# Kernel tuning notes

Measured on AMD Instinct MI355X. Metric: run time of the kernel, lower is better.

Reference implementation:

```python
import jax, jax.numpy as jnp
import numpy as np

N_NODES = 100000
N_EDGES = 1600000
IN_DIM, HID_DIM, OUT_DIM = 32, 16, 8


def setup_inputs() -> dict:
    key = jax.random.key(0)
    ks = jax.random.split(key, 10)
    x = jax.random.normal(ks[0], (N_NODES, IN_DIM), dtype=jnp.float32)
    edge_index = jax.random.randint(ks[1], (2, N_EDGES), 0, N_NODES, dtype=jnp.int32)
    s1 = 1.0 / np.sqrt(IN_DIM)
    s2 = 1.0 / np.sqrt(HID_DIM)
    s3 = 1.0 / np.sqrt(OUT_DIM)
    return {
        "x": x,
        "edge_index": edge_index,
        # SAGEConv layer 1: lin_l (neighbor, with bias) and lin_r (root)
        "Wl1": jax.random.uniform(ks[2], (HID_DIM, IN_DIM), jnp.float32, -s1, s1),
        "bl1": jnp.zeros((HID_DIM,), jnp.float32),
        "Wr1": jax.random.uniform(ks[3], (HID_DIM, IN_DIM), jnp.float32, -s1, s1),
        # SAGEConv layer 2
        "Wl2": jax.random.uniform(ks[4], (OUT_DIM, HID_DIM), jnp.float32, -s2, s2),
        "bl2": jnp.zeros((OUT_DIM,), jnp.float32),
        "Wr2": jax.random.uniform(ks[5], (OUT_DIM, HID_DIM), jnp.float32, -s2, s2),
        # final Linear head
        "Wfc": jax.random.uniform(ks[6], (1, OUT_DIM), jnp.float32, -s3, s3),
        "bfc": jax.random.uniform(ks[7], (1,), jnp.float32, -s3, s3),
    }


def _sage_conv(x, src, dst, Wl, bl, Wr):
    # mean-aggregate neighbor messages x[src] at destination nodes
    msg_sum = jax.ops.segment_sum(x[src], dst, num_segments=N_NODES)  # [N, d]
    deg = jax.ops.segment_sum(jnp.ones((src.shape[0],), x.dtype), dst, num_segments=N_NODES)
    mean = msg_sum / jnp.maximum(deg, 1.0)[:, None]
    # out = lin_l(mean_neighbors) + lin_r(x_root)
    return mean @ Wl.T + bl + x @ Wr.T


def reference(x, edge_index, Wl1, bl1, Wr1, Wl2, bl2, Wr2, Wfc, bfc):
    src, dst = edge_index[0], edge_index[1]
    h = _sage_conv(x, src, dst, Wl1, bl1, Wr1)
    h = jax.nn.relu(h)
    h = _sage_conv(h, src, dst, Wl2, bl2, Wr2)
    return h @ Wfc.T + bfc  # [N, 1]
```

## Files before the change

kernel.cpp:

```cpp
#include <hip/hip_runtime.h>

#define NN 100000
#define NE 1600000
#define IN_DIM 32
#define HID_DIM 16
#define OUT_DIM 8

#define NPB 256
#define NBK ((NN + NPB - 1) / NPB)
#define CAP 5632
#define EPB 4096
#define NT_BUCKET ((NE + EPB - 1) / EPB)
#define NT_PRE1 ((NN + 255) / 256)
#define GRID1 (NT_BUCKET + NT_PRE1)
#define BF_STRIDE 16

__global__ __launch_bounds__(256) void k_phase1(
    const float* __restrict__ x, const int* __restrict__ src, const int* __restrict__ dst,
    const float* __restrict__ Wl1, const float* __restrict__ bl1, const float* __restrict__ Wr1,
    const float* __restrict__ Wl2, const float* __restrict__ bl2, const float* __restrict__ Wr2,
    const float* __restrict__ Wfc, const float* __restrict__ bfc,
    int* __restrict__ bucketfill, unsigned int* __restrict__ bucket,
    float* __restrict__ z, float* __restrict__ rb, float* __restrict__ uvc)
{
    __shared__ char smemraw[4800];
    int tid = threadIdx.x;

    if (blockIdx.x < NT_BUCKET) {
        int* lcnt  = (int*)smemraw;
        int* lbase = lcnt + NBK;
        int* lfill = lbase + NBK;
        int e0 = blockIdx.x * EPB;
        int e1 = min(e0 + EPB, NE);
        for (int i = tid; i < NBK; i += 256) lcnt[i] = 0;
        __syncthreads();
        for (int e = e0 + tid; e < e1; e += 256) atomicAdd(&lcnt[dst[e] >> 8], 1);
        __syncthreads();
        for (int i = tid; i < NBK; i += 256) {
            lbase[i] = (lcnt[i] > 0) ? atomicAdd(&bucketfill[i * BF_STRIDE], lcnt[i]) : 0;
            lfill[i] = 0;
        }
        __syncthreads();
        for (int e = e0 + tid; e < e1; e += 256) {
            int d = dst[e], s = src[e];
            int b = d >> 8;
            int p = atomicAdd(&lfill[b], 1);
            bucket[(size_t)b * CAP + lbase[b] + p] =
                (unsigned)(d & (NPB - 1)) | ((unsigned)s << 8);
        }
    } else {
        int chunk = blockIdx.x - NT_BUCKET;
        float* sWl = (float*)smemraw;
        float* sWr = sWl + 512;
        float* sb  = sWr + 512;
        for (int i = tid; i < HID_DIM * IN_DIM; i += 256) {
            sWl[i] = Wl1[i];
            sWr[i] = Wr1[i];
        }
        if (tid < HID_DIM) sb[tid] = bl1[tid];
        if (chunk == 0) {
            if (tid < HID_DIM) {
                float uu = 0.f, vv = 0.f;
#pragma unroll
                for (int o = 0; o < OUT_DIM; o++) {
                    uu += Wfc[o] * Wl2[o * HID_DIM + tid];
                    vv += Wfc[o] * Wr2[o * HID_DIM + tid];
                }
                uvc[tid] = uu;
                uvc[HID_DIM + tid] = vv;
            }
            if (tid == 0) {
                float c0 = bfc[0];
#pragma unroll
                for (int o = 0; o < OUT_DIM; o++) c0 += Wfc[o] * bl2[o];
                uvc[2 * HID_DIM] = c0;
            }
        }
        __syncthreads();
        int n = chunk * 256 + tid;
        if (n < NN) {
            float xv[IN_DIM];
            const float4* x4 = (const float4*)(x + (size_t)n * IN_DIM);
#pragma unroll
            for (int c = 0; c < 8; c++) {
                float4 b = x4[c];
                xv[c * 4 + 0] = b.x; xv[c * 4 + 1] = b.y;
                xv[c * 4 + 2] = b.z; xv[c * 4 + 3] = b.w;
            }
            float zo[HID_DIM], ro[HID_DIM];
#pragma unroll
            for (int o = 0; o < HID_DIM; o++) {
                float az = 0.f, ar = sb[o];
#pragma unroll
                for (int i = 0; i < IN_DIM; i++) {
                    az += sWl[o * IN_DIM + i] * xv[i];
                    ar += sWr[o * IN_DIM + i] * xv[i];
                }
                zo[o] = az; ro[o] = ar;
            }
            float4* z4 = (float4*)(z + (size_t)n * HID_DIM);
            float4* r4 = (float4*)(rb + (size_t)n * HID_DIM);
#pragma unroll
            for (int c = 0; c < 4; c++) {
                z4[c] = make_float4(zo[c*4], zo[c*4+1], zo[c*4+2], zo[c*4+3]);
                r4[c] = make_float4(ro[c*4], ro[c*4+1], ro[c*4+2], ro[c*4+3]);
            }
        }
    }
}

__global__ __launch_bounds__(256) void k_sort_gather(
    const int* __restrict__ bucketfill, const unsigned int* __restrict__ bucket,
    const float* __restrict__ z, const float* __restrict__ rb, const float* __restrict__ uvc,
    int* __restrict__ deg, int* __restrict__ rowstart, int* __restrict__ srcs,
    float* __restrict__ sv, float* __restrict__ tv)
{
    __shared__ int lcnt[NPB];
    __shared__ int lscan[NPB];
    __shared__ int lfill[NPB];
    __shared__ int lred[NPB];
    __shared__ int ssrc[CAP];

    int b = blockIdx.x;
    int tid = threadIdx.x;

    int part = 0;
    for (int i = tid; i < b; i += 256) part += bucketfill[i * BF_STRIDE];
    lred[tid] = part;
    __syncthreads();
    for (int off = 128; off > 0; off >>= 1) {
        if (tid < off) lred[tid] += lred[tid + off];
        __syncthreads();
    }
    int base = lred[0];
    int cntb = bucketfill[b * BF_STRIDE];
    const unsigned int* bk = bucket + (size_t)b * CAP;

    lcnt[tid] = 0;
    __syncthreads();
    for (int i = tid; i < cntb; i += 256) atomicAdd(&lcnt[bk[i] & (NPB - 1)], 1);
    __syncthreads();
    lscan[tid] = lcnt[tid];
    __syncthreads();
    for (int off = 1; off < 256; off <<= 1) {
        int tvv = (tid >= off) ? lscan[tid - off] : 0;
        __syncthreads();
        lscan[tid] += tvv;
        __syncthreads();
    }
    int excl = lscan[tid] - lcnt[tid];
    lfill[tid] = excl;
    int node = b * NPB + tid;
    if (node < NN) { deg[node] = lcnt[tid]; rowstart[node] = base + excl; }
    __syncthreads();
    for (int i = tid; i < cntb; i += 256) {
        unsigned v = bk[i];
        int d = v & (NPB - 1);
        int p = atomicAdd(&lfill[d], 1);
        int s = (int)(v >> 8);
        ssrc[p] = s;
        srcs[base + p] = s;
    }
    __syncthreads();

    int c = tid & 3;
    int nl0 = tid >> 2;
    float4 u4 = ((const float4*)uvc)[c];
    float4 v4 = ((const float4*)uvc)[4 + c];
#pragma unroll
    for (int pass = 0; pass < 4; pass++) {
        int nl = pass * 64 + nl0;
        int n2 = b * NPB + nl;
        if (n2 < NN) {
            int dg = lcnt[nl];
            int st = lscan[nl] - dg;
            float4 acc = {0.f, 0.f, 0.f, 0.f};
            for (int i = 0; i < dg; i++) {
                int sc = ssrc[st + i];
                float4 vz = ((const float4*)z)[sc * 4 + c];
                acc.x += vz.x; acc.y += vz.y; acc.z += vz.z; acc.w += vz.w;
            }
            float inv = 1.0f / fmaxf((float)dg, 1.0f);
            float4 r = ((const float4*)rb)[n2 * 4 + c];
            float h0 = fmaxf(acc.x * inv + r.x, 0.f);
            float h1 = fmaxf(acc.y * inv + r.y, 0.f);
            float h2 = fmaxf(acc.z * inv + r.z, 0.f);
            float h3 = fmaxf(acc.w * inv + r.w, 0.f);
            float ps = u4.x * h0 + u4.y * h1 + u4.z * h2 + u4.w * h3;
            float pt = v4.x * h0 + v4.y * h1 + v4.z * h2 + v4.w * h3;
            ps += __shfl_xor(ps, 1);
            ps += __shfl_xor(ps, 2);
            pt += __shfl_xor(pt, 1);
            pt += __shfl_xor(pt, 2);
            if (c == 0) { sv[n2] = ps; tv[n2] = pt; }
        }
    }
}

__global__ __launch_bounds__(256) void k_final(
    const int* __restrict__ srcs, const int* __restrict__ deg, const int* __restrict__ rowstart,
    const float* __restrict__ sv, const float* __restrict__ tv,
    const float* __restrict__ uvc, float* __restrict__ out)
{
    int v = blockIdx.x * 256 + threadIdx.x;
    if (v >= NN * 4) return;
    int n = v >> 2;
    int c = v & 3;
    int dg = deg[n];
    int st = rowstart[n];
    float acc = 0.f;
    for (int i = c; i < dg; i += 4) acc += sv[srcs[st + i]];
    acc += __shfl_xor(acc, 1);
    acc += __shfl_xor(acc, 2);
    if (c == 0) out[n] = acc / fmaxf((float)dg, 1.0f) + tv[n] + uvc[2 * HID_DIM];
}

extern "C" void kernel_launch(void* const* d_in, const int* in_sizes, int n_in,
                              void* d_out, int out_size, void* d_ws, size_t ws_size,
                              hipStream_t stream) {
    const float* x   = (const float*)d_in[0];
    const int*   ei  = (const int*)d_in[1];
    const float* Wl1 = (const float*)d_in[2];
    const float* bl1 = (const float*)d_in[3];
    const float* Wr1 = (const float*)d_in[4];
    const float* Wl2 = (const float*)d_in[5];
    const float* bl2 = (const float*)d_in[6];
    const float* Wr2 = (const float*)d_in[7];
    const float* Wfc = (const float*)d_in[8];
    const float* bfc = (const float*)d_in[9];
    float* out = (float*)d_out;

    const int* src = ei;
    const int* dst = ei + NE;

    int* bucketfill = (int*)d_ws;
    int* deg        = bucketfill + 6400;
    int* rowstart   = deg + NN;
    int* srcs       = rowstart + NN;
    float* uvc      = (float*)(srcs + NE);
    float* sv       = uvc + 40;
    float* tv       = sv + NN;
    unsigned int* bucket = (unsigned int*)(tv + NN);
    float* z        = (float*)(bucket + (size_t)NBK * CAP);
    float* rb       = z + (size_t)NN * HID_DIM;

    hipMemsetAsync(bucketfill, 0, NBK * BF_STRIDE * sizeof(int), stream);

    k_phase1<<<GRID1, 256, 0, stream>>>(x, src, dst, Wl1, bl1, Wr1,
                                        Wl2, bl2, Wr2, Wfc, bfc,
                                        bucketfill, bucket, z, rb, uvc);
    k_sort_gather<<<NBK, 256, 0, stream>>>(bucketfill, bucket, z, rb, uvc,
                                           deg, rowstart, srcs, sv, tv);
    k_final<<<((NN * 4) + 255) / 256, 256, 0, stream>>>(srcs, deg, rowstart, sv, tv, uvc, out);
}
```

Measured before the change: 164.0 us.

## Locally sort edges by bucket in LDS before coalesced bucket scatter

The bucketing pass now keeps dst values in registers, runs an exclusive prefix scan over per-bucket counts, and places the packed edges in shared memory sorted by bucket. They are then written to the global buckets in sorted order, so neighbouring threads write to contiguous addresses instead of scattering at random. In exchange it adds two 256-wide Hillis-Steele scans with many barriers and about 26KB of static LDS per block, which may lower occupancy for the precompute blocks that share the kernel. The scan assumes NBK is at most 512.

```diff
diff --git a/kernel.cpp b/kernel.cpp
--- a/kernel.cpp
+++ b/kernel.cpp
@@ -10,6 +10,7 @@
 #define NBK ((NN + NPB - 1) / NPB)
 #define CAP 5632
 #define EPB 4096
+#define EPT (EPB / 256)
 #define NT_BUCKET ((NE + EPB - 1) / EPB)
 #define NT_PRE1 ((NN + 255) / 256)
 #define GRID1 (NT_BUCKET + NT_PRE1)
@@ -23,36 +24,84 @@
     int* __restrict__ bucketfill, unsigned int* __restrict__ bucket,
     float* __restrict__ z, float* __restrict__ rb, float* __restrict__ uvc)
 {
-    __shared__ char smemraw[4800];
+    __shared__ int lcnt[NBK];
+    __shared__ int lpos[NBK];
+    __shared__ int lbase[NBK];
+    __shared__ int lfill[NBK];
+    __shared__ int sscan[256];
+    __shared__ unsigned int ssorted[EPB];
+    __shared__ unsigned short sbin[EPB];
     int tid = threadIdx.x;
 
     if (blockIdx.x < NT_BUCKET) {
-        int* lcnt  = (int*)smemraw;
-        int* lbase = lcnt + NBK;
-        int* lfill = lbase + NBK;
         int e0 = blockIdx.x * EPB;
         int e1 = min(e0 + EPB, NE);
+        int total = e1 - e0;
+
         for (int i = tid; i < NBK; i += 256) lcnt[i] = 0;
         __syncthreads();
-        for (int e = e0 + tid; e < e1; e += 256) atomicAdd(&lcnt[dst[e] >> 8], 1);
-        __syncthreads();
+
+        int myd[EPT];
+#pragma unroll
+        for (int k = 0; k < EPT; k++) {
+            int e = e0 + k * 256 + tid;
+            myd[k] = (e < e1) ? dst[e] : -1;
+            if (myd[k] >= 0) atomicAdd(&lcnt[myd[k] >> 8], 1);
+        }
+        __syncthreads();
+
+        int vA = lcnt[tid];
+        sscan[tid] = vA;
+        __syncthreads();
+        for (int off = 1; off < 256; off <<= 1) {
+            int t2 = (tid >= off) ? sscan[tid - off] : 0;
+            __syncthreads();
+            sscan[tid] += t2;
+            __syncthreads();
+        }
+        int totalA = sscan[255];
+        lpos[tid] = sscan[tid] - vA;
+        __syncthreads();
+        int vB = (tid < NBK - 256) ? lcnt[256 + tid] : 0;
+        sscan[tid] = vB;
+        __syncthreads();
+        for (int off = 1; off < 256; off <<= 1) {
+            int t2 = (tid >= off) ? sscan[tid - off] : 0;
+            __syncthreads();
+            sscan[tid] += t2;
+            __syncthreads();
+        }
+        if (tid < NBK - 256) lpos[256 + tid] = totalA + sscan[tid] - vB;
+        __syncthreads();
+
         for (int i = tid; i < NBK; i += 256) {
             lbase[i] = (lcnt[i] > 0) ? atomicAdd(&bucketfill[i * BF_STRIDE], lcnt[i]) : 0;
-            lfill[i] = 0;
-        }
-        __syncthreads();
-        for (int e = e0 + tid; e < e1; e += 256) {
-            int d = dst[e], s = src[e];
-            int b = d >> 8;
-            int p = atomicAdd(&lfill[b], 1);
-            bucket[(size_t)b * CAP + lbase[b] + p] =
-                (unsigned)(d & (NPB - 1)) | ((unsigned)s << 8);
+            lfill[i] = lpos[i];
+        }
+        __syncthreads();
+
+#pragma unroll
+        for (int k = 0; k < EPT; k++) {
+            if (myd[k] >= 0) {
+                int e = e0 + k * 256 + tid;
+                int s = src[e];
+                int b = myd[k] >> 8;
+                int p = atomicAdd(&lfill[b], 1);
+                ssorted[p] = (unsigned)(myd[k] & (NPB - 1)) | ((unsigned)s << 8);
+                sbin[p] = (unsigned short)b;
+            }
+        }
+        __syncthreads();
+
+        for (int i = tid; i < total; i += 256) {
+            int b = sbin[i];
+            bucket[(size_t)b * CAP + lbase[b] + (i - lpos[b])] = ssorted[i];
         }
     } else {
         int chunk = blockIdx.x - NT_BUCKET;
-        float* sWl = (float*)smemraw;
+        float* sWl = (float*)ssorted;
         float* sWr = sWl + 512;
-        float* sb  = sWr + 512;
+        float* sb  = (float*)sbin;
         for (int i = tid; i < HID_DIM * IN_DIM; i += 256) {
             sWl[i] = Wl1[i];
             sWr[i] = Wr1[i];
```

New measurement: 164.3 us. Within noise of the previous version (+0.2%).
